# Optimization experiments

Measured on AMD Instinct MI355X. Metric: run time of the kernel, lower is better.

## Reference

```python
import jax, jax.numpy as jnp
import numpy as np

TOP_K = 2
AUX_COEF = 1e-3

def setup_inputs() -> dict:
    key = jax.random.key(0)
    ks = jax.random.split(key, 5)
    B, S, H, I, E = 4, 2048, 1024, 2048, 8
    x = jax.random.normal(ks[0], (B, S, H), jnp.float32)
    gate_w = jax.random.normal(ks[1], (H, E), jnp.float32) * 0.02
    w_gate = jax.random.normal(ks[2], (E, H, I), jnp.float32) * 0.02
    w_up = jax.random.normal(ks[3], (E, H, I), jnp.float32) * 0.02
    w_down = jax.random.normal(ks[4], (E, I, H), jnp.float32) * 0.02
    return {"x": x, "gate_w": gate_w, "w_gate": w_gate, "w_up": w_up, "w_down": w_down}


def reference(x, gate_w, w_gate, w_up, w_down):
    B, S, H = x.shape
    E = gate_w.shape[1]
    xf = x.reshape(-1, H)              # [N, H]
    N = xf.shape[0]

    # Router: softmax in fp32 (matches F.softmax(..., dtype=torch.float32))
    logits = xf @ gate_w               # [N, E]
    rw = jax.nn.softmax(logits.astype(jnp.float32), axis=-1).astype(x.dtype)
    top_w, top_i = jax.lax.top_k(rw, TOP_K)            # [N, K]
    top_w = top_w / top_w.sum(axis=-1, keepdims=True)  # renormalize

    # Combine weights: comb[t, e] = sum_k top_w[t,k] * (top_i[t,k]==e)
    comb = jnp.zeros((N, E), x.dtype).at[jnp.arange(N)[:, None], top_i].add(top_w)

    # SwiGLU FFN computed densely per expert, masked/combined by router weights
    h_gate = jax.nn.silu(jnp.einsum('th,ehi->eti', xf, w_gate))   # [E, N, I]
    h_up = jnp.einsum('th,ehi->eti', xf, w_up)                    # [E, N, I]
    expert_out = jnp.einsum('eti,eih->eth', h_gate * h_up, w_down)  # [E, N, H]
    y = jnp.einsum('eth,te->th', expert_out, comb).reshape(B, S, H)

    # Load-balancing aux loss
    sel_w = jnp.take_along_axis(rw, top_i, axis=1)   # router weight of chosen experts [N, K]
    load = jnp.zeros((E,), rw.dtype).at[top_i.reshape(-1)].add(sel_w.reshape(-1))
    P_expert = load / N
    counts = jnp.zeros((E,), jnp.float32).at[top_i.reshape(-1)].add(1.0)
    P_token_expert = counts / (N * TOP_K)
    aux_loss = (P_expert * P_token_expert).sum() * E * AUX_COEF
    return y, aux_loss
```

## Files before the change

### kernel.cpp

```cpp
#include <hip/hip_runtime.h>

#define N_TOK 8192
#define H_DIM 1024
#define I_DIM 2048
#define N_EXP 8
#define TOPK  2
#define CAP   18432
#define MT_MAX 72

#define OFF_TOPK_I 0u
#define OFF_TOPK_W 65536u
#define OFF_COUNTS 131072u
#define OFF_LOAD   131104u
#define OFF_CURSOR 131136u
#define OFF_PO     131168u
#define OFF_TILE_E 131232u
#define OFF_BTOK   131744u
#define OFF_BW     205472u
#define CTRL_BYTES 279200u
#define OFF_TSLOT  279552u
#define OFF_WGT  1048576u
#define OFF_WUT  (OFF_WGT + 33554432u)
#define OFF_WDT  (OFF_WUT + 33554432u)
#define OFF_HB   (OFF_WDT + 33554432u)
#define OFF_XB   (OFF_HB + 75497472u)

typedef __attribute__((ext_vector_type(8))) short bf16x8;
typedef __attribute__((ext_vector_type(8))) unsigned short u16x8;
typedef __attribute__((ext_vector_type(4))) unsigned short u16x4;
typedef __attribute__((ext_vector_type(4))) float f32x4;

#define BAR() __builtin_amdgcn_s_barrier()
#define PRIO1() __builtin_amdgcn_s_setprio(1)
#define PRIO0() __builtin_amdgcn_s_setprio(0)
#define WAITV0() asm volatile("s_waitcnt vmcnt(0)" ::: "memory")
#define WAITV6() asm volatile("s_waitcnt vmcnt(6)" ::: "memory")

__device__ __forceinline__ unsigned short f2bf(float f) {
  union { float f; unsigned int u; } v; v.f = f;
  unsigned int r = (v.u + 0x7FFFu + ((v.u >> 16) & 1u)) >> 16;
  return (unsigned short)r;
}
__device__ __forceinline__ float bf2f(unsigned short u) {
  union { unsigned int u; float f; } v; v.u = ((unsigned int)u) << 16;
  return v.f;
}
__device__ __forceinline__ u16x8 pack8(float4 a, float4 b) {
  u16x8 r;
  r[0] = f2bf(a.x); r[1] = f2bf(a.y); r[2] = f2bf(a.z); r[3] = f2bf(a.w);
  r[4] = f2bf(b.x); r[5] = f2bf(b.y); r[6] = f2bf(b.z); r[7] = f2bf(b.w);
  return r;
}
__device__ __forceinline__ f32x4 mfma32(bf16x8 a, bf16x8 b, f32x4 c) {
  return __builtin_amdgcn_mfma_f32_16x16x32_bf16(a, b, c, 0, 0, 0);
}
__device__ __forceinline__ void gll16(const void* g, void* l) {
  __builtin_amdgcn_global_load_lds(
      (const __attribute__((address_space(1))) unsigned int*)g,
      (__attribute__((address_space(3))) unsigned int*)l, 16, 0, 0);
}

__global__ __launch_bounds__(256) void k_transpose(
    const float* __restrict__ wg, const float* __restrict__ wu, const float* __restrict__ wd,
    unsigned short* __restrict__ wgT, unsigned short* __restrict__ wuT,
    unsigned short* __restrict__ wdT)
{
  __shared__ unsigned short lds[64][65];
  int bid = blockIdx.x;
  int m = bid / 4096; int rem = bid % 4096;
  const float* src; unsigned short* dst; int R, C;
  if (m == 0)      { src = wg; dst = wgT; R = 1024; C = 2048; }
  else if (m == 1) { src = wu; dst = wuT; R = 1024; C = 2048; }
  else             { src = wd; dst = wdT; R = 2048; C = 1024; }
  int e = rem / 512; int trem = rem % 512;
  int tcc = C / 64;
  int r0 = (trem / tcc) * 64, c0 = (trem % tcc) * 64;
  size_t ebase = (size_t)e * R * C;
  dst += ebase;
  int tid = threadIdx.x;
  int lr = tid >> 3;
  int lc = (tid & 7) * 8;
#pragma unroll
  for (int p = 0; p < 2; ++p) {
    int row = p * 32 + lr;
    size_t off = ebase + (size_t)(r0 + row) * C + c0 + lc;
    float4 q0 = *(const float4*)&src[off];
    float4 q1 = *(const float4*)&src[off + 4];
    unsigned short tmp[8]; *(u16x8*)tmp = pack8(q0, q1);
#pragma unroll
    for (int j = 0; j < 8; ++j) lds[row][lc + j] = tmp[j];
  }
  __syncthreads();
#pragma unroll
  for (int p = 0; p < 2; ++p) {
    int drow = p * 32 + lr;
    unsigned short tmp[8];
#pragma unroll
    for (int j = 0; j < 8; ++j) tmp[j] = lds[lc + j][drow];
    *(u16x8*)&dst[(size_t)(c0 + drow) * R + r0 + lc] = *(const u16x8*)tmp;
  }
}

__global__ __launch_bounds__(256) void k_router(
    const float* __restrict__ x, const float* __restrict__ gw,
    unsigned short* __restrict__ xb,
    int* __restrict__ topk_i, float* __restrict__ topk_w)
{
  int wave = threadIdx.x >> 6, lane = threadIdx.x & 63;
  int t = blockIdx.x * 4 + wave;
  const float* xr = x + (size_t)t * H_DIM;
  float acc[8];
#pragma unroll
  for (int e = 0; e < 8; ++e) acc[e] = 0.f;
#pragma unroll
  for (int it = 0; it < H_DIM / 64; ++it) {
    int h = it * 64 + lane;
    float xv = xr[h];
    xb[(size_t)t * H_DIM + h] = f2bf(xv);
    float4 g0 = *(const float4*)&gw[h * 8];
    float4 g1 = *(const float4*)&gw[h * 8 + 4];
    acc[0] += xv * g0.x; acc[1] += xv * g0.y; acc[2] += xv * g0.z; acc[3] += xv * g0.w;
    acc[4] += xv * g1.x; acc[5] += xv * g1.y; acc[6] += xv * g1.z; acc[7] += xv * g1.w;
  }
#pragma unroll
  for (int off = 32; off > 0; off >>= 1) {
#pragma unroll
    for (int e = 0; e < 8; ++e) acc[e] += __shfl_xor(acc[e], off);
  }
  if (lane == 0) {
    float m = acc[0];
#pragma unroll
    for (int e = 1; e < 8; ++e) m = fmaxf(m, acc[e]);
    float p[8], s = 0.f;
#pragma unroll
    for (int e = 0; e < 8; ++e) { p[e] = __expf(acc[e] - m); s += p[e]; }
    float inv = 1.f / s;
#pragma unroll
    for (int e = 0; e < 8; ++e) p[e] *= inv;
    int i1 = 0;
#pragma unroll
    for (int e = 1; e < 8; ++e) if (p[e] > p[i1]) i1 = e;
    int i2 = (i1 == 0) ? 1 : 0;
#pragma unroll
    for (int e = 0; e < 8; ++e) if (e != i1 && p[e] > p[i2]) i2 = e;
    topk_i[t * 2]     = i1; topk_i[t * 2 + 1] = i2;
    topk_w[t * 2]     = p[i1]; topk_w[t * 2 + 1] = p[i2];
  }
}

__global__ __launch_bounds__(256) void k_hist(
    const int* __restrict__ topk_i, const float* __restrict__ topk_w,
    int* __restrict__ counts, float* __restrict__ loadw)
{
  __shared__ int c[8]; __shared__ float l[8];
  int tid = threadIdx.x;
  if (tid < 8) { c[tid] = 0; l[tid] = 0.f; }
  __syncthreads();
  int base = blockIdx.x * 1024 + tid * 4;
#pragma unroll
  for (int j = 0; j < 4; ++j) {
    int e = topk_i[base + j];
    float w = topk_w[base + j];
    atomicAdd(&c[e], 1);
    atomicAdd(&l[e], w);
  }
  __syncthreads();
  if (tid < 8) { atomicAdd(&counts[tid], c[tid]); atomicAdd(&loadw[tid], l[tid]); }
}

__global__ __launch_bounds__(256) void k_offsets(
    const int* __restrict__ counts, const float* __restrict__ loadw,
    int* __restrict__ po, int* __restrict__ tile_e, float* __restrict__ out)
{
  __shared__ int spo[9];
  if (threadIdx.x == 0) {
    int a = 0;
    for (int e = 0; e < 8; ++e) { spo[e] = a; po[e] = a; a += (counts[e] + 255) & ~255; }
    spo[8] = a; po[8] = a;
    float s = 0.f;
    for (int e = 0; e < 8; ++e) s += loadw[e] * (float)counts[e];
    out[(size_t)N_TOK * H_DIM] =
        s * ((float)N_EXP * 1e-3f) / ((float)N_TOK * (float)N_TOK * (float)TOPK);
  }
  __syncthreads();
  int mt = threadIdx.x;
  if (mt < MT_MAX) {
    int te = -1, beg = mt * 256;
    if (beg < spo[8]) {
      for (int e = 0; e < 8; ++e) if (beg >= spo[e] && beg < spo[e + 1]) te = e;
    }
    tile_e[mt] = te;
  }
}

__global__ __launch_bounds__(256) void k_bucket(
    const int* __restrict__ topk_i, const float* __restrict__ topk_w,
    const int* __restrict__ po, int* __restrict__ cursor,
    int* __restrict__ btok, float* __restrict__ bw, int* __restrict__ tslot)
{
  __shared__ int c[8];
  __shared__ int basee[8];
  int tid = threadIdx.x;
  if (tid < 8) c[tid] = 0;
  __syncthreads();
  int base = blockIdx.x * 1024 + tid * 4;
  int e4[4], r4[4]; float w4[4];
#pragma unroll
  for (int j = 0; j < 4; ++j) {
    int idx = base + j;
    int e = topk_i[idx];
    e4[j] = e;
    r4[j] = atomicAdd(&c[e], 1);
    int t = idx >> 1;
    float p0 = topk_w[t * 2], p1 = topk_w[t * 2 + 1];
    w4[j] = topk_w[idx] / (p0 + p1);
  }
  __syncthreads();
  if (tid < 8) basee[tid] = po[tid] + atomicAdd(&cursor[tid], c[tid]);
  __syncthreads();
#pragma unroll
  for (int j = 0; j < 4; ++j) {
    int idx = base + j;
    int slot = basee[e4[j]] + r4[j];
    btok[slot] = idx >> 1;
    bw[slot] = w4[j];
    tslot[idx] = slot;
  }
}

__global__ __launch_bounds__(512, 2) void k_gemm1(
    const unsigned short* __restrict__ xb,
    const unsigned short* __restrict__ wgT, const unsigned short* __restrict__ wuT,
    const int* __restrict__ btok, const int* __restrict__ tile_e,
    unsigned short* __restrict__ hbuf)
{
  int nt = blockIdx.x, mt = blockIdx.y;
  int e = tile_e[mt];
  if (e < 0) return;
  __shared__ unsigned char smem[131072];
  unsigned short* lds = (unsigned short*)smem;
  float* uex = (float*)smem;
  int tid = threadIdx.x;
  int wave = tid >> 6, lane = tid & 63;
  int grp = wave >> 2;
  int g4 = wave & 3;
  int wm = g4 >> 1, wn = g4 & 1;
  int quad = lane >> 4, l16 = lane & 15;
  int lsw = l16 & 7;

  const unsigned short* srcA[4]; unsigned dstA[4];
#pragma unroll
  for (int c = 0; c < 4; ++c) {
    int idx = c * 512 + wave * 64 + lane;
    int row = idx >> 3;
    int ch  = (idx & 7) ^ (row & 7);
    int tok = btok[mt * 256 + row];
    srcA[c] = xb + (size_t)tok * H_DIM + ch * 8;
    dstA[c] = (unsigned)(c * 512 + wave * 64) * 8;
  }
  const unsigned short* srcG[2]; const unsigned short* srcU[2]; unsigned dstB[2];
#pragma unroll
  for (int c = 0; c < 2; ++c) {
    int idx = c * 512 + wave * 64 + lane;
    int col = idx >> 3;
    int ch  = (idx & 7) ^ (col & 7);
    srcG[c] = wgT + ((size_t)e * I_DIM + nt * 128 + col) * H_DIM + ch * 8;
    srcU[c] = wuT + ((size_t)e * I_DIM + nt * 128 + col) * H_DIM + ch * 8;
    dstB[c] = (unsigned)(c * 512 + wave * 64) * 8;
  }
  unsigned boff = grp ? 24576u : 16384u;

  f32x4 acc[8][4];
  f32x4 z = {0.f, 0.f, 0.f, 0.f};
#pragma unroll
  for (int i = 0; i < 8; ++i)
#pragma unroll
    for (int j = 0; j < 4; ++j) acc[i][j] = z;

#pragma unroll
  for (int c = 0; c < 4; ++c) gll16(srcA[c], &lds[dstA[c]]);
#pragma unroll
  for (int c = 0; c < 2; ++c) {
    gll16(srcG[c], &lds[16384u + dstB[c]]);
    gll16(srcU[c], &lds[24576u + dstB[c]]);
  }
  WAITV0();
  BAR();

  for (int t = 0; t < 16; ++t) {
    unsigned bo  = (unsigned)(t & 1) * 32768u;
    unsigned bo1 = bo ^ 32768u;
    if (t < 15) {
      int kel = (t + 1) * 64;
#pragma unroll
      for (int c = 0; c < 4; ++c) gll16(srcA[c] + kel, &lds[bo1 + dstA[c]]);
#pragma unroll
      for (int c = 0; c < 2; ++c) {
        gll16(srcG[c] + kel, &lds[bo1 + 16384u + dstB[c]]);
        gll16(srcU[c] + kel, &lds[bo1 + 24576u + dstB[c]]);
      }
    }
    PRIO1();
#pragma unroll
    for (int ks = 0; ks < 2; ++ks) {
      bf16x8 b[4];
#pragma unroll
      for (int nf = 0; nf < 4; ++nf) {
        unsigned col = (unsigned)(wn * 64 + nf * 16 + l16);
        b[nf] = *(const bf16x8*)&lds[bo + boff + col * 64 + (unsigned)(((ks * 4 + quad) ^ lsw) * 8)];
      }
#pragma unroll
      for (int mf = 0; mf < 8; ++mf) {
        unsigned row = (unsigned)(wm * 128 + mf * 16 + l16);
        bf16x8 a = *(const bf16x8*)&lds[bo + row * 64 + (unsigned)(((ks * 4 + quad) ^ lsw) * 8)];
#pragma unroll
        for (int nf = 0; nf < 4; ++nf) acc[mf][nf] = mfma32(a, b[nf], acc[mf][nf]);
      }
    }
    PRIO0();
    WAITV0();
    BAR();
  }

  if (grp == 1) {
#pragma unroll
    for (int mf = 0; mf < 8; ++mf)
#pragma unroll
      for (int r = 0; r < 4; ++r) {
        int row = wm * 128 + mf * 16 + quad * 4 + r;
#pragma unroll
        for (int nf = 0; nf < 4; ++nf)
          uex[row * 128 + wn * 64 + nf * 16 + l16] = acc[mf][nf][r];
      }
  }
  BAR();
  if (grp == 0) {
#pragma unroll
    for (int mf = 0; mf < 8; ++mf)
#pragma unroll
      for (int r = 0; r < 4; ++r) {
        int row = wm * 128 + mf * 16 + quad * 4 + r;
        size_t base = (size_t)(mt * 256 + row) * I_DIM + nt * 128;
#pragma unroll
        for (int nf = 0; nf < 4; ++nf) {
          float g = acc[mf][nf][r];
          float u = uex[row * 128 + wn * 64 + nf * 16 + l16];
          float sg = g / (1.f + __expf(-g));
          hbuf[base + wn * 64 + nf * 16 + l16] = f2bf(sg * u);
        }
      }
  }
}

__global__ __launch_bounds__(512, 2) void k_gemm2(
    const unsigned short* __restrict__ hbuf, const unsigned short* __restrict__ wdT,
    const int* __restrict__ tile_e, unsigned short* __restrict__ obuf)
{
  int mt = blockIdx.y, nt = blockIdx.x;
  int e = tile_e[mt];
  if (e < 0) return;
  __shared__ unsigned short lds[73728];
  int tid = threadIdx.x;
  int wave = tid >> 6, lane = tid & 63;
  int wm = wave >> 2, wn = wave & 3;
  int quad = lane >> 4, l16 = lane & 15;

  int rp = lane >> 3;
  int chunk = (lane & 7) ^ rp;
  const unsigned short* sA[2][2]; const unsigned short* sB[2];
  unsigned dA[2][2], dB[2];
#pragma unroll
  for (int h = 0; h < 2; ++h)
#pragma unroll
    for (int c = 0; c < 2; ++c) {
      int rowp = wave * 16 + c * 8 + rp;
      sA[h][c] = hbuf + (size_t)(mt * 256 + h * 128 + rowp) * I_DIM + chunk * 8;
      dA[h][c] = (unsigned)(h * 128 + wave * 16 + c * 8) * 64;
    }
#pragma unroll
  for (int c = 0; c < 2; ++c) {
    int rowp = wave * 16 + c * 8 + rp;
    sB[c] = wdT + ((size_t)e * H_DIM + nt * 128 + rowp) * I_DIM + chunk * 8;
    dB[c] = (unsigned)(wave * 16 + c * 8) * 64;
  }

  f32x4 acc[8][2];
  f32x4 z = {0.f, 0.f, 0.f, 0.f};
#pragma unroll
  for (int i = 0; i < 8; ++i) { acc[i][0] = z; acc[i][1] = z; }

  int fsw = l16 & 7;
#pragma unroll
  for (int tt = 0; tt < 2; ++tt) {
    unsigned bo = (unsigned)tt * 24576;
    int kel = tt * 64;
#pragma unroll
    for (int h = 0; h < 2; ++h)
#pragma unroll
      for (int c = 0; c < 2; ++c) gll16(sA[h][c] + kel, &lds[bo + dA[h][c]]);
#pragma unroll
    for (int c = 0; c < 2; ++c) gll16(sB[c] + kel, &lds[bo + 16384 + dB[c]]);
  }
  WAITV6();
  BAR();

  unsigned boA = 0, boB = 24576, boC = 49152;
  for (int t = 0; t < 32; ++t) {
    int kel = (t + 2) * 64;
    bool pf = (t < 30);
    bf16x8 b[2][2];
#pragma unroll
    for (int nf = 0; nf < 2; ++nf)
#pragma unroll
      for (int ks = 0; ks < 2; ++ks) {
        int col = wn * 32 + nf * 16 + l16;
        b[nf][ks] = *(const bf16x8*)&lds[boA + 16384 + col * 64 + (((ks * 4 + quad) ^ fsw) * 8)];
      }
    {
      bf16x8 a[4][2];
#pragma unroll
      for (int m = 0; m < 4; ++m)
#pragma unroll
        for (int ks = 0; ks < 2; ++ks) {
          int row = wm * 128 + m * 16 + l16;
          a[m][ks] = *(const bf16x8*)&lds[boA + row * 64 + (((ks * 4 + quad) ^ fsw) * 8)];
        }
      if (pf) {
#pragma unroll
        for (int h = 0; h < 2; ++h)
#pragma unroll
          for (int c = 0; c < 2; ++c) gll16(sA[h][c] + kel, &lds[boC + dA[h][c]]);
      }
      BAR();
      PRIO1();
#pragma unroll
      for (int m = 0; m < 4; ++m)
#pragma unroll
        for (int nf = 0; nf < 2; ++nf)
#pragma unroll
          for (int ks = 0; ks < 2; ++ks) acc[m][nf] = mfma32(a[m][ks], b[nf][ks], acc[m][nf]);
      PRIO0();
      BAR();
    }
    {
      bf16x8 a[4][2];
#pragma unroll
      for (int m = 0; m < 4; ++m)
#pragma unroll
        for (int ks = 0; ks < 2; ++ks) {
          int row = wm * 128 + (4 + m) * 16 + l16;
          a[m][ks] = *(const bf16x8*)&lds[boA + row * 64 + (((ks * 4 + quad) ^ fsw) * 8)];
        }
      if (pf) {
#pragma unroll
        for (int c = 0; c < 2; ++c) gll16(sB[c] + kel, &lds[boC + 16384 + dB[c]]);
      }
      BAR();
      PRIO1();
#pragma unroll
      for (int m = 0; m < 4; ++m)
#pragma unroll
        for (int nf = 0; nf < 2; ++nf)
#pragma unroll
          for (int ks = 0; ks < 2; ++ks) acc[4 + m][nf] = mfma32(a[m][ks], b[nf][ks], acc[4 + m][nf]);
      PRIO0();
    }
    if (pf) { WAITV6(); } else { WAITV0(); }
    BAR();
    unsigned tmp = boA; boA = boB; boB = boC; boC = tmp;
  }
#pragma unroll
  for (int m = 0; m < 8; ++m)
#pragma unroll
    for (int r = 0; r < 4; ++r) {
      int s = mt * 256 + wm * 128 + m * 16 + quad * 4 + r;
      size_t base = (size_t)s * H_DIM + nt * 128 + wn * 32 + l16;
      obuf[base]      = f2bf(acc[m][0][r]);
      obuf[base + 16] = f2bf(acc[m][1][r]);
    }
}

__global__ __launch_bounds__(256) void k_final(
    const unsigned short* __restrict__ obuf, const int* __restrict__ tslot,
    const float* __restrict__ bw, float* __restrict__ y)
{
  int t = blockIdx.x;
  int s0 = tslot[t * 2], s1 = tslot[t * 2 + 1];
  float w0 = bw[s0], w1 = bw[s1];
  int c = threadIdx.x * 4;
  u16x4 o0 = *(const u16x4*)&obuf[(size_t)s0 * H_DIM + c];
  u16x4 o1 = *(const u16x4*)&obuf[(size_t)s1 * H_DIM + c];
  float4 r;
  r.x = w0 * bf2f(o0[0]) + w1 * bf2f(o1[0]);
  r.y = w0 * bf2f(o0[1]) + w1 * bf2f(o1[1]);
  r.z = w0 * bf2f(o0[2]) + w1 * bf2f(o1[2]);
  r.w = w0 * bf2f(o0[3]) + w1 * bf2f(o1[3]);
  *(float4*)&y[(size_t)t * H_DIM + c] = r;
}

extern "C" void kernel_launch(void* const* d_in, const int* in_sizes, int n_in,
                              void* d_out, int out_size, void* d_ws, size_t ws_size,
                              hipStream_t stream)
{
  (void)in_sizes; (void)n_in; (void)out_size; (void)ws_size;
  const float* x  = (const float*)d_in[0];
  const float* gw = (const float*)d_in[1];
  const float* wg = (const float*)d_in[2];
  const float* wu = (const float*)d_in[3];
  const float* wd = (const float*)d_in[4];
  char* ws = (char*)d_ws;

  int*   topk_i = (int*)  (ws + OFF_TOPK_I);
  float* topk_w = (float*)(ws + OFF_TOPK_W);
  int*   counts = (int*)  (ws + OFF_COUNTS);
  float* loadw  = (float*)(ws + OFF_LOAD);
  int*   cursor = (int*)  (ws + OFF_CURSOR);
  int*   po     = (int*)  (ws + OFF_PO);
  int*   tile_e = (int*)  (ws + OFF_TILE_E);
  int*   btok   = (int*)  (ws + OFF_BTOK);
  float* bw     = (float*)(ws + OFF_BW);
  int*   tslot  = (int*)  (ws + OFF_TSLOT);
  unsigned short* wgT  = (unsigned short*)(ws + OFF_WGT);
  unsigned short* wuT  = (unsigned short*)(ws + OFF_WUT);
  unsigned short* wdT  = (unsigned short*)(ws + OFF_WDT);
  unsigned short* hbuf = (unsigned short*)(ws + OFF_HB);
  unsigned short* xb   = (unsigned short*)(ws + OFF_XB);
  unsigned short* obuf = (unsigned short*)(ws + OFF_WGT);
  float* yout = (float*)d_out;

  (void)hipMemsetAsync(ws, 0, CTRL_BYTES, stream);
  k_router<<<N_TOK / 4, 256, 0, stream>>>(x, gw, xb, topk_i, topk_w);
  k_transpose<<<12288, 256, 0, stream>>>(wg, wu, wd, wgT, wuT, wdT);
  k_hist<<<16, 256, 0, stream>>>(topk_i, topk_w, counts, loadw);
  k_offsets<<<1, 256, 0, stream>>>(counts, loadw, po, tile_e, (float*)d_out);
  k_bucket<<<16, 256, 0, stream>>>(topk_i, topk_w, po, cursor, btok, bw, tslot);
  k_gemm1<<<dim3(I_DIM / 128, MT_MAX), 512, 0, stream>>>(xb, wgT, wuT, btok, tile_e, hbuf);
  k_gemm2<<<dim3(H_DIM / 128, MT_MAX), 512, 0, stream>>>(hbuf, wdT, tile_e, obuf);
  k_final<<<N_TOK, 256, 0, stream>>>(obuf, tslot, bw, yout);
}
```

Baseline: 561.2 us.

## Switch GEMMs to 32x32x16 MFMA and fuse router into transpose kernel

Both expert GEMMs move from 16x16x32 bf16 MFMA to 32x32x16 bf16 MFMA. The LDS fragment offsets are precomputed and the accumulator layout and epilogue indexing are remapped to match. This cuts the number of LDS fragment reads per MFMA FLOP and the instruction count. The router kernel is merged into the weight transpose/convert kernel as extra blocks to save a launch and let both overlap, and it now reads x with float4 loads. The changes risk register pressure from the f32x16 accumulators and possible LDS bank conflicts under the new access pattern.

```diff
diff --git a/kernel.cpp b/kernel.cpp
--- a/kernel.cpp
+++ b/kernel.cpp
@@ -29,6 +29,7 @@
 typedef __attribute__((ext_vector_type(8))) unsigned short u16x8;
 typedef __attribute__((ext_vector_type(4))) unsigned short u16x4;
 typedef __attribute__((ext_vector_type(4))) float f32x4;
+typedef __attribute__((ext_vector_type(16))) float f32x16;
 
 #define BAR() __builtin_amdgcn_s_barrier()
 #define PRIO1() __builtin_amdgcn_s_setprio(1)
@@ -51,8 +52,8 @@
   r[4] = f2bf(b.x); r[5] = f2bf(b.y); r[6] = f2bf(b.z); r[7] = f2bf(b.w);
   return r;
 }
-__device__ __forceinline__ f32x4 mfma32(bf16x8 a, bf16x8 b, f32x4 c) {
-  return __builtin_amdgcn_mfma_f32_16x16x32_bf16(a, b, c, 0, 0, 0);
+__device__ __forceinline__ f32x16 mfma3216(bf16x8 a, bf16x8 b, f32x16 c) {
+  return __builtin_amdgcn_mfma_f32_32x32x16_bf16(a, b, c, 0, 0, 0);
 }
 __device__ __forceinline__ void gll16(const void* g, void* l) {
   __builtin_amdgcn_global_load_lds(
@@ -60,13 +61,64 @@
       (__attribute__((address_space(3))) unsigned int*)l, 16, 0, 0);
 }
 
-__global__ __launch_bounds__(256) void k_transpose(
+__global__ __launch_bounds__(256) void k_prep(
+    const float* __restrict__ x, const float* __restrict__ gw,
     const float* __restrict__ wg, const float* __restrict__ wu, const float* __restrict__ wd,
+    unsigned short* __restrict__ xb,
     unsigned short* __restrict__ wgT, unsigned short* __restrict__ wuT,
-    unsigned short* __restrict__ wdT)
+    unsigned short* __restrict__ wdT,
+    int* __restrict__ topk_i, float* __restrict__ topk_w)
 {
   __shared__ unsigned short lds[64][65];
-  int bid = blockIdx.x;
+  if (blockIdx.x < 2048) {
+    int wave = threadIdx.x >> 6, lane = threadIdx.x & 63;
+    int t = blockIdx.x * 4 + wave;
+    const float4* xr4 = (const float4*)(x + (size_t)t * H_DIM);
+    float acc[8];
+#pragma unroll
+    for (int e = 0; e < 8; ++e) acc[e] = 0.f;
+#pragma unroll
+    for (int it = 0; it < 4; ++it) {
+      int hq = it * 64 + lane;
+      float4 xv = xr4[hq];
+      u16x4 xo; xo[0] = f2bf(xv.x); xo[1] = f2bf(xv.y); xo[2] = f2bf(xv.z); xo[3] = f2bf(xv.w);
+      *(u16x4*)&xb[(size_t)t * H_DIM + hq * 4] = xo;
+      float xs[4] = {xv.x, xv.y, xv.z, xv.w};
+#pragma unroll
+      for (int j = 0; j < 4; ++j) {
+        float4 g0 = *(const float4*)&gw[(hq * 4 + j) * 8];
+        float4 g1 = *(const float4*)&gw[(hq * 4 + j) * 8 + 4];
+        acc[0] += xs[j] * g0.x; acc[1] += xs[j] * g0.y; acc[2] += xs[j] * g0.z; acc[3] += xs[j] * g0.w;
+        acc[4] += xs[j] * g1.x; acc[5] += xs[j] * g1.y; acc[6] += xs[j] * g1.z; acc[7] += xs[j] * g1.w;
+      }
+    }
+#pragma unroll
+    for (int off = 32; off > 0; off >>= 1) {
+#pragma unroll
+      for (int e = 0; e < 8; ++e) acc[e] += __shfl_xor(acc[e], off);
+    }
+    if (lane == 0) {
+      float m = acc[0];
+#pragma unroll
+      for (int e = 1; e < 8; ++e) m = fmaxf(m, acc[e]);
+      float p[8], s = 0.f;
+#pragma unroll
+      for (int e = 0; e < 8; ++e) { p[e] = __expf(acc[e] - m); s += p[e]; }
+      float inv = 1.f / s;
+#pragma unroll
+      for (int e = 0; e < 8; ++e) p[e] *= inv;
+      int i1 = 0;
+#pragma unroll
+      for (int e = 1; e < 8; ++e) if (p[e] > p[i1]) i1 = e;
+      int i2 = (i1 == 0) ? 1 : 0;
+#pragma unroll
+      for (int e = 0; e < 8; ++e) if (e != i1 && p[e] > p[i2]) i2 = e;
+      topk_i[t * 2]     = i1; topk_i[t * 2 + 1] = i2;
+      topk_w[t * 2]     = p[i1]; topk_w[t * 2 + 1] = p[i2];
+    }
+    return;
+  }
+  int bid = blockIdx.x - 2048;
   int m = bid / 4096; int rem = bid % 4096;
   const float* src; unsigned short* dst; int R, C;
   if (m == 0)      { src = wg; dst = wgT; R = 1024; C = 2048; }
@@ -101,53 +153,6 @@
   }
 }
 
-__global__ __launch_bounds__(256) void k_router(
-    const float* __restrict__ x, const float* __restrict__ gw,
-    unsigned short* __restrict__ xb,
-    int* __restrict__ topk_i, float* __restrict__ topk_w)
-{
-  int wave = threadIdx.x >> 6, lane = threadIdx.x & 63;
-  int t = blockIdx.x * 4 + wave;
-  const float* xr = x + (size_t)t * H_DIM;
-  float acc[8];
-#pragma unroll
-  for (int e = 0; e < 8; ++e) acc[e] = 0.f;
-#pragma unroll
-  for (int it = 0; it < H_DIM / 64; ++it) {
-    int h = it * 64 + lane;
-    float xv = xr[h];
-    xb[(size_t)t * H_DIM + h] = f2bf(xv);
-    float4 g0 = *(const float4*)&gw[h * 8];
-    float4 g1 = *(const float4*)&gw[h * 8 + 4];
-    acc[0] += xv * g0.x; acc[1] += xv * g0.y; acc[2] += xv * g0.z; acc[3] += xv * g0.w;
-    acc[4] += xv * g1.x; acc[5] += xv * g1.y; acc[6] += xv * g1.z; acc[7] += xv * g1.w;
-  }
-#pragma unroll
-  for (int off = 32; off > 0; off >>= 1) {
-#pragma unroll
-    for (int e = 0; e < 8; ++e) acc[e] += __shfl_xor(acc[e], off);
-  }
-  if (lane == 0) {
-    float m = acc[0];
-#pragma unroll
-    for (int e = 1; e < 8; ++e) m = fmaxf(m, acc[e]);
-    float p[8], s = 0.f;
-#pragma unroll
-    for (int e = 0; e < 8; ++e) { p[e] = __expf(acc[e] - m); s += p[e]; }
-    float inv = 1.f / s;
-#pragma unroll
-    for (int e = 0; e < 8; ++e) p[e] *= inv;
-    int i1 = 0;
-#pragma unroll
-    for (int e = 1; e < 8; ++e) if (p[e] > p[i1]) i1 = e;
-    int i2 = (i1 == 0) ? 1 : 0;
-#pragma unroll
-    for (int e = 0; e < 8; ++e) if (e != i1 && p[e] > p[i2]) i2 = e;
-    topk_i[t * 2]     = i1; topk_i[t * 2 + 1] = i2;
-    topk_w[t * 2]     = p[i1]; topk_w[t * 2 + 1] = p[i2];
-  }
-}
-
 __global__ __launch_bounds__(256) void k_hist(
     const int* __restrict__ topk_i, const float* __restrict__ topk_w,
     int* __restrict__ counts, float* __restrict__ loadw)
@@ -245,8 +250,7 @@
   int grp = wave >> 2;
   int g4 = wave & 3;
   int wm = g4 >> 1, wn = g4 & 1;
-  int quad = lane >> 4, l16 = lane & 15;
-  int lsw = l16 & 7;
+  int l32 = lane & 31, half = lane >> 5;
 
   const unsigned short* srcA[4]; unsigned dstA[4];
 #pragma unroll
@@ -268,14 +272,27 @@
     srcU[c] = wuT + ((size_t)e * I_DIM + nt * 128 + col) * H_DIM + ch * 8;
     dstB[c] = (unsigned)(c * 512 + wave * 64) * 8;
   }
-  unsigned boff = grp ? 24576u : 16384u;
-
-  f32x4 acc[8][4];
-  f32x4 z = {0.f, 0.f, 0.f, 0.f};
-#pragma unroll
-  for (int i = 0; i < 8; ++i)
-#pragma unroll
-    for (int j = 0; j < 4; ++j) acc[i][j] = z;
+  unsigned breg = grp ? 24576u : 16384u;
+
+  unsigned aofs[4][4], bofs[2][4];
+#pragma unroll
+  for (int mf = 0; mf < 4; ++mf)
+#pragma unroll
+    for (int ks = 0; ks < 4; ++ks)
+      aofs[mf][ks] = (unsigned)(wm * 128 + mf * 32 + l32) * 64 +
+                     ((((unsigned)ks * 2 + half) ^ (unsigned)(lane & 7)) * 8);
+#pragma unroll
+  for (int nf = 0; nf < 2; ++nf)
+#pragma unroll
+    for (int ks = 0; ks < 4; ++ks)
+      bofs[nf][ks] = breg + (unsigned)(wn * 64 + nf * 32 + l32) * 64 +
+                     ((((unsigned)ks * 2 + half) ^ (unsigned)(lane & 7)) * 8);
+
+  f32x16 acc[4][2];
+#pragma unroll
+  for (int i = 0; i < 4; ++i)
+#pragma unroll
+    for (int j = 0; j < 2; ++j) acc[i][j] = (f32x16)0.f;
 
 #pragma unroll
   for (int c = 0; c < 4; ++c) gll16(srcA[c], &lds[dstA[c]]);
@@ -302,19 +319,14 @@
     }
     PRIO1();
 #pragma unroll
-    for (int ks = 0; ks < 2; ++ks) {
-      bf16x8 b[4];
-#pragma unroll
-      for (int nf = 0; nf < 4; ++nf) {
-        unsigned col = (unsigned)(wn * 64 + nf * 16 + l16);
-        b[nf] = *(const bf16x8*)&lds[bo + boff + col * 64 + (unsigned)(((ks * 4 + quad) ^ lsw) * 8)];
-      }
-#pragma unroll
-      for (int mf = 0; mf < 8; ++mf) {
-        unsigned row = (unsigned)(wm * 128 + mf * 16 + l16);
-        bf16x8 a = *(const bf16x8*)&lds[bo + row * 64 + (unsigned)(((ks * 4 + quad) ^ lsw) * 8)];
-#pragma unroll
-        for (int nf = 0; nf < 4; ++nf) acc[mf][nf] = mfma32(a, b[nf], acc[mf][nf]);
+    for (int ks = 0; ks < 4; ++ks) {
+      bf16x8 b0 = *(const bf16x8*)&lds[bo + bofs[0][ks]];
+      bf16x8 b1 = *(const bf16x8*)&lds[bo + bofs[1][ks]];
+#pragma unroll
+      for (int mf = 0; mf < 4; ++mf) {
+        bf16x8 a = *(const bf16x8*)&lds[bo + aofs[mf][ks]];
+        acc[mf][0] = mfma3216(a, b0, acc[mf][0]);
+        acc[mf][1] = mfma3216(a, b1, acc[mf][1]);
       }
     }
     PRIO0();
@@ -324,29 +336,29 @@
 
   if (grp == 1) {
 #pragma unroll
-    for (int mf = 0; mf < 8; ++mf)
-#pragma unroll
-      for (int r = 0; r < 4; ++r) {
-        int row = wm * 128 + mf * 16 + quad * 4 + r;
-#pragma unroll
-        for (int nf = 0; nf < 4; ++nf)
-          uex[row * 128 + wn * 64 + nf * 16 + l16] = acc[mf][nf][r];
+    for (int mf = 0; mf < 4; ++mf)
+#pragma unroll
+      for (int rr = 0; rr < 16; ++rr) {
+        int row = wm * 128 + mf * 32 + (rr & 3) + 8 * (rr >> 2) + 4 * half;
+#pragma unroll
+        for (int nf = 0; nf < 2; ++nf)
+          uex[row * 128 + wn * 64 + nf * 32 + l32] = acc[mf][nf][rr];
       }
   }
   BAR();
   if (grp == 0) {
 #pragma unroll
-    for (int mf = 0; mf < 8; ++mf)
-#pragma unroll
-      for (int r = 0; r < 4; ++r) {
-        int row = wm * 128 + mf * 16 + quad * 4 + r;
+    for (int mf = 0; mf < 4; ++mf)
+#pragma unroll
+      for (int rr = 0; rr < 16; ++rr) {
+        int row = wm * 128 + mf * 32 + (rr & 3) + 8 * (rr >> 2) + 4 * half;
         size_t base = (size_t)(mt * 256 + row) * I_DIM + nt * 128;
 #pragma unroll
-        for (int nf = 0; nf < 4; ++nf) {
-          float g = acc[mf][nf][r];
-          float u = uex[row * 128 + wn * 64 + nf * 16 + l16];
+        for (int nf = 0; nf < 2; ++nf) {
+          float g = acc[mf][nf][rr];
+          float u = uex[row * 128 + wn * 64 + nf * 32 + l32];
           float sg = g / (1.f + __expf(-g));
-          hbuf[base + wn * 64 + nf * 16 + l16] = f2bf(sg * u);
+          hbuf[base + wn * 64 + nf * 32 + l32] = f2bf(sg * u);
         }
       }
   }
@@ -363,7 +375,7 @@
   int tid = threadIdx.x;
   int wave = tid >> 6, lane = tid & 63;
   int wm = wave >> 2, wn = wave & 3;
-  int quad = lane >> 4, l16 = lane & 15;
+  int l32 = lane & 31, half = lane >> 5;
 
   int rp = lane >> 3;
   int chunk = (lane & 7) ^ rp;
@@ -384,12 +396,22 @@
     dB[c] = (unsigned)(wave * 16 + c * 8) * 64;
   }
 
-  f32x4 acc[8][2];
-  f32x4 z = {0.f, 0.f, 0.f, 0.f};
-#pragma unroll
-  for (int i = 0; i < 8; ++i) { acc[i][0] = z; acc[i][1] = z; }
-
-  int fsw = l16 & 7;
+  unsigned aofs[4][4], bofs[4];
+#pragma unroll
+  for (int mf = 0; mf < 4; ++mf)
+#pragma unroll
+    for (int ks = 0; ks < 4; ++ks)
+      aofs[mf][ks] = (unsigned)(wm * 128 + mf * 32 + l32) * 64 +
+                     ((((unsigned)ks * 2 + half) ^ (unsigned)(lane & 7)) * 8);
+#pragma unroll
+  for (int ks = 0; ks < 4; ++ks)
+    bofs[ks] = 16384u + (unsigned)(wn * 32 + l32) * 64 +
+               ((((unsigned)ks * 2 + half) ^ (unsigned)(lane & 7)) * 8);
+
+  f32x16 acc[4];
+#pragma unroll
+  for (int i = 0; i < 4; ++i) acc[i] = (f32x16)0.f;
+
 #pragma unroll
   for (int tt = 0; tt < 2; ++tt) {
     unsigned bo = (unsigned)tt * 24576;
@@ -408,23 +430,16 @@
   for (int t = 0; t < 32; ++t) {
     int kel = (t + 2) * 64;
     bool pf = (t < 30);
-    bf16x8 b[2][2];
-#pragma unroll
-    for (int nf = 0; nf < 2; ++nf)
-#pragma unroll
-      for (int ks = 0; ks < 2; ++ks) {
-        int col = wn * 32 + nf * 16 + l16;
-        b[nf][ks] = *(const bf16x8*)&lds[boA + 16384 + col * 64 + (((ks * 4 + quad) ^ fsw) * 8)];
-      }
+    bf16x8 b[4];
+#pragma unroll
+    for (int ks = 0; ks < 4; ++ks) b[ks] = *(const bf16x8*)&lds[boA + bofs[ks]];
     {
       bf16x8 a[4][2];
 #pragma unroll
-      for (int m = 0; m < 4; ++m)
-#pragma unroll
-        for (int ks = 0; ks < 2; ++ks) {
-          int row = wm * 128 + m * 16 + l16;
-          a[m][ks] = *(const bf16x8*)&lds[boA + row * 64 + (((ks * 4 + quad) ^ fsw) * 8)];
-        }
+      for (int mf = 0; mf < 4; ++mf)
+#pragma unroll
+        for (int ks = 0; ks < 2; ++ks)
+          a[mf][ks] = *(const bf16x8*)&lds[boA + aofs[mf][ks]];
       if (pf) {
 #pragma unroll
         for (int h = 0; h < 2; ++h)
@@ -434,23 +449,19 @@
       BAR();
       PRIO1();
 #pragma unroll
-      for (int m = 0; m < 4; ++m)
-#pragma unroll
-        for (int nf = 0; nf < 2; ++nf)
-#pragma unroll
-          for (int ks = 0; ks < 2; ++ks) acc[m][nf] = mfma32(a[m][ks], b[nf][ks], acc[m][nf]);
+      for (int mf = 0; mf < 4; ++mf)
+#pragma unroll
+        for (int ks = 0; ks < 2; ++ks) acc[mf] = mfma3216(a[mf][ks], b[ks], acc[mf]);
       PRIO0();
       BAR();
     }
     {
       bf16x8 a[4][2];
 #pragma unroll
-      for (int m = 0; m < 4; ++m)
-#pragma unroll
-        for (int ks = 0; ks < 2; ++ks) {
-          int row = wm * 128 + (4 + m) * 16 + l16;
-          a[m][ks] = *(const bf16x8*)&lds[boA + row * 64 + (((ks * 4 + quad) ^ fsw) * 8)];
-        }
+      for (int mf = 0; mf < 4; ++mf)
+#pragma unroll
+        for (int ks = 0; ks < 2; ++ks)
+          a[mf][ks] = *(const bf16x8*)&lds[boA + aofs[mf][2 + ks]];
       if (pf) {
 #pragma unroll
         for (int c = 0; c < 2; ++c) gll16(sB[c] + kel, &lds[boC + 16384 + dB[c]]);
@@ -458,11 +469,9 @@
       BAR();
       PRIO1();
 #pragma unroll
-      for (int m = 0; m < 4; ++m)
-#pragma unroll
-        for (int nf = 0; nf < 2; ++nf)
-#pragma unroll
-          for (int ks = 0; ks < 2; ++ks) acc[4 + m][nf] = mfma32(a[m][ks], b[nf][ks], acc[4 + m][nf]);
+      for (int mf = 0; mf < 4; ++mf)
+#pragma unroll
+        for (int ks = 0; ks < 2; ++ks) acc[mf] = mfma3216(a[mf][ks], b[2 + ks], acc[mf]);
       PRIO0();
     }
     if (pf) { WAITV6(); } else { WAITV0(); }
@@ -470,13 +479,11 @@
     unsigned tmp = boA; boA = boB; boB = boC; boC = tmp;
   }
 #pragma unroll
-  for (int m = 0; m < 8; ++m)
-#pragma unroll
-    for (int r = 0; r < 4; ++r) {
-      int s = mt * 256 + wm * 128 + m * 16 + quad * 4 + r;
-      size_t base = (size_t)s * H_DIM + nt * 128 + wn * 32 + l16;
-      obuf[base]      = f2bf(acc[m][0][r]);
-      obuf[base + 16] = f2bf(acc[m][1][r]);
+  for (int mf = 0; mf < 4; ++mf)
+#pragma unroll
+    for (int rr = 0; rr < 16; ++rr) {
+      int s = mt * 256 + wm * 128 + mf * 32 + (rr & 3) + 8 * (rr >> 2) + 4 * half;
+      obuf[(size_t)s * H_DIM + nt * 128 + wn * 32 + l32] = f2bf(acc[mf][rr]);
     }
 }
 
@@ -529,8 +536,7 @@
   float* yout = (float*)d_out;
 
   (void)hipMemsetAsync(ws, 0, CTRL_BYTES, stream);
-  k_router<<<N_TOK / 4, 256, 0, stream>>>(x, gw, xb, topk_i, topk_w);
-  k_transpose<<<12288, 256, 0, stream>>>(wg, wu, wd, wgT, wuT, wdT);
+  k_prep<<<14336, 256, 0, stream>>>(x, gw, wg, wu, wd, xb, wgT, wuT, wdT, topk_i, topk_w);
   k_hist<<<16, 256, 0, stream>>>(topk_i, topk_w, counts, loadw);
   k_offsets<<<1, 256, 0, stream>>>(counts, loadw, po, tile_e, (float*)d_out);
   k_bucket<<<16, 256, 0, stream>>>(topk_i, topk_w, po, cursor, btok, bw, tslot);
```

Result: slower. 585.4 us (+4.3%).
